# Kernel tuning notes

Hardware: AMD Instinct MI355X
Metric: run time of the kernel (lower is better)

## Reference

```python
import jax, jax.numpy as jnp
import numpy as np
from jax import lax

NUM_LAYERS = 128
SEQ_LEN = 256
H = 1  # hidden_size = input_size = 1


def setup_inputs() -> dict:
    key = jax.random.key(0)
    k = jax.random.split(key, 5)
    # PyTorch GRU init: U(-1/sqrt(H), 1/sqrt(H)) with H=1 -> U(-1, 1)
    u = lambda kk, shp: jax.random.uniform(kk, shp, jnp.float32, -1.0, 1.0)
    return {
        "x": jax.random.normal(k[0], (1, SEQ_LEN), jnp.float32),
        "w_ih": u(k[1], (NUM_LAYERS, 3 * H, H)),  # gates stacked [r, z, n]
        "w_hh": u(k[2], (NUM_LAYERS, 3 * H, H)),
        "b_ih": u(k[3], (NUM_LAYERS, 3 * H)),
        "b_hh": u(k[4], (NUM_LAYERS, 3 * H)),
    }


def _gru_stack(x_seq, w_ih, w_hh, b_ih, b_hh):
    # x_seq: [T, H]; params stacked over layers. PyTorch GRU equations, gate order r,z,n.
    def layer_step(seq, params):
        wi, wh, bi, bh = params  # [3H,H], [3H,H], [3H], [3H]

        def cell(h, xt):  # h: [H], xt: [H]
            gi = wi @ xt + bi  # [3H]
            gh = wh @ h + bh   # [3H]
            r = jax.nn.sigmoid(gi[0:H] + gh[0:H])
            z = jax.nn.sigmoid(gi[H:2 * H] + gh[H:2 * H])
            n = jnp.tanh(gi[2 * H:] + r * gh[2 * H:])
            h_new = (1.0 - z) * n + z * h
            return h_new, h_new

        h0 = jnp.zeros((H,), dtype=seq.dtype)
        _, out = lax.scan(cell, h0, seq)  # out: [T, H]
        return out, None

    out, _ = lax.scan(layer_step, x_seq, (w_ih, w_hh, b_ih, b_hh))
    return out


def reference(x, w_ih, w_hh, b_ih, b_hh):
    # x: [1, T] -> GRU input [T, H=1] (unbatched), encoder only (decoder unused in forward)
    seq = x.T  # [T, 1]
    out = _gru_stack(seq, w_ih, w_hh, b_ih, b_hh)  # [T, 1]
    return out.T  # [1, T]
```

## Files before the change

### kernel.cpp

```cpp
#include <hip/hip_runtime.h>

#define T_LEN 256
#define NG 26

__device__ __forceinline__ float ex2(float x) { return __builtin_amdgcn_exp2f(x); }
__device__ __forceinline__ float rcp1p(float e) { return __builtin_amdgcn_rcpf(1.0f + e); }

__device__ __forceinline__ float dpp_wave_shr1(float v) {
    int i = __float_as_int(v);
    return __int_as_float(__builtin_amdgcn_update_dpp(i, i, 0x138, 0xF, 0xF, false));
}
__device__ __forceinline__ float dpp_wave_rol1(float v) {
    int i = __float_as_int(v);
    return __int_as_float(__builtin_amdgcn_update_dpp(i, i, 0x134, 0xF, 0xF, false));
}

__global__ __launch_bounds__(128, 1) void gru_stack_wavefront(
    const float* __restrict__ x,
    const float* __restrict__ w_ih,
    const float* __restrict__ w_hh,
    const float* __restrict__ b_ih,
    const float* __restrict__ b_hh,
    float* __restrict__ out)
{
    __shared__ float ring[2 * 64 * 64];
    const int tid  = threadIdx.x;
    const int lane = tid & 63;
    const int wid  = tid >> 6;

    #pragma unroll 4
    for (int m = tid; m < 2 * 64 * 64; m += 128) ring[m] = 0.0f;

    const float L1 = -1.4426950408889634f;
    const float L2 = -2.8853900817779268f;

    const float wi_r = L1 * w_ih[3 * tid + 0], wh_r = L1 * w_hh[3 * tid + 0];
    const float b_r  = L1 * (b_ih[3 * tid + 0] + b_hh[3 * tid + 0]);
    const float wi_z = L1 * w_ih[3 * tid + 1], wh_z = L1 * w_hh[3 * tid + 1];
    const float b_z  = L1 * (b_ih[3 * tid + 1] + b_hh[3 * tid + 1]);
    const float wi_n = L2 * w_ih[3 * tid + 2], bi_n = L2 * b_ih[3 * tid + 2];
    const float wh_n = L2 * w_hh[3 * tid + 2], bh_n = L2 * b_hh[3 * tid + 2];

    float xc0 = x[lane];
    float xc1 = x[lane + 64];
    float xc2 = x[lane + 128];
    float xc3 = x[lane + 192];

    float h = 0.0f;
    float c_r = b_r, c_z = b_z, g_n = bh_n;

    float pcur[16], pnext[16];
    #pragma unroll
    for (int k = 0; k < 16; ++k) { pcur[k] = 0.0f; pnext[k] = 0.0f; }

    float ov = 0.0f;
    float xq = xc0;
    int t = -lane - 96 * wid - 1;

    const bool is_l0 = (lane == 0);
    const bool is_w1 = (wid == 1);
    float* ringw = &ring[wid * 4096];

    __syncthreads();

    for (int g = 0; g < NG; ++g) {
        if      (g == 4)  xq = xc1;
        else if (g == 8)  xq = xc2;
        else if (g == 12) xq = xc3;

        if (is_w1) {
            const int base = 16 * g - 17;
            #pragma unroll
            for (int k = 0; k < 16; ++k)
                pnext[k] = ring[((base + k) & 63) * 64 + 63];
        }

        const int sb = (16 * g) & 63;

        #pragma unroll
        for (int k = 0; k < 16; ++k) {
            ++t;
            const bool valid = (unsigned)t < (unsigned)T_LEN;

            float alt = is_w1 ? pcur[k] : xq;
            float shifted = dpp_wave_shr1(h);
            float in = is_l0 ? alt : shifted;

            float u_r  = fmaf(wi_r, in, c_r);
            float u_z  = fmaf(wi_z, in, c_z);
            float u_n0 = fmaf(wi_n, in, bi_n);
            float r = rcp1p(ex2(u_r));
            float z = rcp1p(ex2(u_z));
            z = valid ? z : 1.0f;
            float two_omz = fmaf(-2.0f, z, 2.0f);
            float zh_m    = fmaf(z, h, z - 1.0f);
            float s_n = rcp1p(ex2(fmaf(r, g_n, u_n0)));
            h = fmaf(s_n, two_omz, zh_m);

            c_r = fmaf(wh_r, h, b_r);
            c_z = fmaf(wh_z, h, b_z);
            g_n = fmaf(wh_n, h, bh_n);

            ringw[((sb + k) & 63) * 64 + lane] = h;

            float rot = dpp_wave_rol1(ov);
            ov = (lane == 63) ? h : rot;
            xq = dpp_wave_rol1(xq);

            if (k == 14) {
                if (is_w1 && (g & 3) == 1 && g >= 13)
                    out[16 * g - 208 + lane] = ov;
            }
        }

        if (is_w1) {
            #pragma unroll
            for (int k = 0; k < 16; ++k) pcur[k] = pnext[k];
        }
        __syncthreads();
    }
}

extern "C" void kernel_launch(void* const* d_in, const int* in_sizes, int n_in,
                              void* d_out, int out_size, void* d_ws, size_t ws_size,
                              hipStream_t stream) {
    const float* x    = (const float*)d_in[0];
    const float* w_ih = (const float*)d_in[1];
    const float* w_hh = (const float*)d_in[2];
    const float* b_ih = (const float*)d_in[3];
    const float* b_hh = (const float*)d_in[4];
    float* out = (float*)d_out;

    gru_stack_wavefront<<<1, 128, 0, stream>>>(x, w_ih, w_hh, b_ih, b_hh, out);
}
```

Baseline: 95.03 us.

## Spread GRU layer wavefront across eight waves with 16-lane rows

Result: slower. 126.5 us (+33.2%).

```diff
diff --git a/kernel.cpp b/kernel.cpp
--- a/kernel.cpp
+++ b/kernel.cpp
@@ -1,21 +1,22 @@
 #include <hip/hip_runtime.h>
 
 #define T_LEN 256
-#define NG 26
+#define NG 31
+#define K_SKEW 31
 
 __device__ __forceinline__ float ex2(float x) { return __builtin_amdgcn_exp2f(x); }
 __device__ __forceinline__ float rcp1p(float e) { return __builtin_amdgcn_rcpf(1.0f + e); }
 
-__device__ __forceinline__ float dpp_wave_shr1(float v) {
+__device__ __forceinline__ float dpp_row_shr1(float v) {
     int i = __float_as_int(v);
-    return __int_as_float(__builtin_amdgcn_update_dpp(i, i, 0x138, 0xF, 0xF, false));
+    return __int_as_float(__builtin_amdgcn_update_dpp(i, i, 0x111, 0xF, 0xF, false));
 }
 __device__ __forceinline__ float dpp_wave_rol1(float v) {
     int i = __float_as_int(v);
     return __int_as_float(__builtin_amdgcn_update_dpp(i, i, 0x134, 0xF, 0xF, false));
 }
 
-__global__ __launch_bounds__(128, 1) void gru_stack_wavefront(
+__global__ __launch_bounds__(512, 1) void gru_stack_wavefront(
     const float* __restrict__ x,
     const float* __restrict__ w_ih,
     const float* __restrict__ w_hh,
@@ -23,68 +24,63 @@
     const float* __restrict__ b_hh,
     float* __restrict__ out)
 {
-    __shared__ float ring[2 * 64 * 64];
+    __shared__ float plane[8][64 * 16];
+    __shared__ float sx[T_LEN];
     const int tid  = threadIdx.x;
     const int lane = tid & 63;
-    const int wid  = tid >> 6;
+    const int wv   = tid >> 6;
+    const int j    = lane & 15;
+    const int L    = 16 * wv + j;
 
-    #pragma unroll 4
-    for (int m = tid; m < 2 * 64 * 64; m += 128) ring[m] = 0.0f;
+    if (tid < T_LEN) sx[tid] = x[tid];
+    #pragma unroll
+    for (int m = tid; m < 8 * 64 * 16; m += 512) (&plane[0][0])[m] = 0.0f;
 
     const float L1 = -1.4426950408889634f;
     const float L2 = -2.8853900817779268f;
 
-    const float wi_r = L1 * w_ih[3 * tid + 0], wh_r = L1 * w_hh[3 * tid + 0];
-    const float b_r  = L1 * (b_ih[3 * tid + 0] + b_hh[3 * tid + 0]);
-    const float wi_z = L1 * w_ih[3 * tid + 1], wh_z = L1 * w_hh[3 * tid + 1];
-    const float b_z  = L1 * (b_ih[3 * tid + 1] + b_hh[3 * tid + 1]);
-    const float wi_n = L2 * w_ih[3 * tid + 2], bi_n = L2 * b_ih[3 * tid + 2];
-    const float wh_n = L2 * w_hh[3 * tid + 2], bh_n = L2 * b_hh[3 * tid + 2];
-
-    float xc0 = x[lane];
-    float xc1 = x[lane + 64];
-    float xc2 = x[lane + 128];
-    float xc3 = x[lane + 192];
+    const float wi_r = L1 * w_ih[3 * L + 0], wh_r = L1 * w_hh[3 * L + 0];
+    const float b_r  = L1 * (b_ih[3 * L + 0] + b_hh[3 * L + 0]);
+    const float wi_z = L1 * w_ih[3 * L + 1], wh_z = L1 * w_hh[3 * L + 1];
+    const float b_z  = L1 * (b_ih[3 * L + 1] + b_hh[3 * L + 1]);
+    const float wi_n = L2 * w_ih[3 * L + 2], bi_n = L2 * b_ih[3 * L + 2];
+    const float wh_n = L2 * w_hh[3 * L + 2], bh_n = L2 * b_hh[3 * L + 2];
 
     float h = 0.0f;
     float c_r = b_r, c_z = b_z, g_n = bh_n;
 
-    float pcur[16], pnext[16];
-    #pragma unroll
-    for (int k = 0; k < 16; ++k) { pcur[k] = 0.0f; pnext[k] = 0.0f; }
+    float pk[16];
+    float ov = 0.0f;
+    int t = -j - K_SKEW * wv - 1;
 
-    float ov = 0.0f;
-    float xq = xc0;
-    int t = -lane - 96 * wid - 1;
-
-    const bool is_l0 = (lane == 0);
-    const bool is_w1 = (wid == 1);
-    float* ringw = &ring[wid * 4096];
+    const bool is_j0 = (j == 0);
+    const bool is_w0 = (wv == 0);
+    const bool is_w7 = (wv == 7);
+    float* myplane = plane[wv];
+    const float* srcplane = plane[wv == 0 ? 0 : wv - 1];
 
     __syncthreads();
 
     for (int g = 0; g < NG; ++g) {
-        if      (g == 4)  xq = xc1;
-        else if (g == 8)  xq = xc2;
-        else if (g == 12) xq = xc3;
+        const int sb = 16 * g;
 
-        if (is_w1) {
-            const int base = 16 * g - 17;
+        if (is_w0) {
             #pragma unroll
             for (int k = 0; k < 16; ++k)
-                pnext[k] = ring[((base + k) & 63) * 64 + 63];
+                pk[k] = sx[(sb + k) & (T_LEN - 1)];
+        } else {
+            #pragma unroll
+            for (int k = 0; k < 16; ++k)
+                pk[k] = srcplane[((sb + k - 17) & 63) * 16 + 15];
         }
-
-        const int sb = (16 * g) & 63;
 
         #pragma unroll
         for (int k = 0; k < 16; ++k) {
             ++t;
             const bool valid = (unsigned)t < (unsigned)T_LEN;
 
-            float alt = is_w1 ? pcur[k] : xq;
-            float shifted = dpp_wave_shr1(h);
-            float in = is_l0 ? alt : shifted;
+            float shifted = dpp_row_shr1(h);
+            float in = is_j0 ? pk[k] : shifted;
 
             float u_r  = fmaf(wi_r, in, c_r);
             float u_z  = fmaf(wi_z, in, c_z);
@@ -101,21 +97,13 @@
             c_z = fmaf(wh_z, h, b_z);
             g_n = fmaf(wh_n, h, bh_n);
 
-            ringw[((sb + k) & 63) * 64 + lane] = h;
+            myplane[((sb + k) & 63) * 16 + j] = h;
 
             float rot = dpp_wave_rol1(ov);
             ov = (lane == 63) ? h : rot;
-            xq = dpp_wave_rol1(xq);
 
-            if (k == 14) {
-                if (is_w1 && (g & 3) == 1 && g >= 13)
-                    out[16 * g - 208 + lane] = ov;
-            }
-        }
-
-        if (is_w1) {
-            #pragma unroll
-            for (int k = 0; k < 16; ++k) pcur[k] = pnext[k];
+            if (k == 7 && is_w7 && g >= 18 && ((g - 18) & 3) == 0)
+                out[sb - 288 + lane] = ov;
         }
         __syncthreads();
     }
@@ -131,5 +119,5 @@
     const float* b_hh = (const float*)d_in[4];
     float* out = (float*)d_out;
 
-    gru_stack_wavefront<<<1, 128, 0, stream>>>(x, w_ih, w_hh, b_ih, b_hh, out);
+    gru_stack_wavefront<<<1, 512, 0, stream>>>(x, w_ih, w_hh, b_ih, b_hh, out);
 }
```
